# Kernel tuning notes

Hardware: AMD Instinct MI355X
Metric: run time of the kernel (lower is better)

The kernel has to match this reference:

```python
import jax, jax.numpy as jnp
import numpy as np

N_NODES = 100000
N_EDGES = 1600000
NFEAT = 64
NHID = 64
NCLASS = 16


def setup_inputs() -> dict:
    key = jax.random.key(0)
    k_x, k_e, k_w1, k_b1, k_w2, k_b2 = jax.random.split(key, 6)
    x = jax.random.normal(k_x, (N_NODES, NFEAT), dtype=jnp.float32)
    edge_index = jax.random.randint(k_e, (2, N_EDGES), 0, N_NODES, dtype=jnp.int64)
    # Glorot-ish init for the GIN update MLP
    W1 = jax.random.normal(k_w1, (NFEAT, NHID), dtype=jnp.float32) * (1.0 / np.sqrt(NFEAT))
    b1 = jnp.zeros((NHID,), dtype=jnp.float32)
    W2 = jax.random.normal(k_w2, (NHID, NCLASS), dtype=jnp.float32) * (1.0 / np.sqrt(NHID))
    b2 = jnp.zeros((NCLASS,), dtype=jnp.float32)
    eps = jnp.float32(0.0)  # train_eps=True, initialized to 0
    return {"x": x, "edge_index": edge_index, "eps": eps,
            "W1": W1, "b1": b1, "W2": W2, "b2": b2}


def reference(x, edge_index, eps, W1, b1, W2, b2):
    # GINConv: out = MLP((1 + eps) * x + sum_{j in N(i)} x_j)
    src = edge_index[0]  # message source nodes
    dst = edge_index[1]  # aggregation targets (source_to_target flow)
    agg = jax.ops.segment_sum(x[src], dst, num_segments=x.shape[0])  # [N, F]
    h = (1.0 + eps) * x + agg
    # MLP([nfeat, nhid, nclass]): Linear -> ReLU -> (dropout=identity in eval) -> Linear
    h = jax.nn.relu(h @ W1 + b1)
    return h @ W2 + b2
```

## Files before the change

kernel.cpp:

```cpp
#include <hip/hip_runtime.h>
#include <hip/hip_bf16.h>
#include <hip/hip_fp16.h>


#define NFEAT 64
#define NHID 64
#define NCLASS 16

#define BNODES 128
#define PCAP 2560
#define MAXBUCK 1024
#define PT 512
#define PEPT 8
#define FT 512
#define SEPT 5

__global__ __launch_bounds__(256) void k_tofp16(
    const float4* __restrict__ x4, uint2* __restrict__ xh2, int n16)
{
    int i = blockIdx.x * 256 + threadIdx.x;
    if (i >= n16) return;
    float4 v = x4[i];
    __half2 a = __floats2half2_rn(v.x, v.y);
    __half2 b = __floats2half2_rn(v.z, v.w);
    xh2[i] = make_uint2(*(unsigned*)&a, *(unsigned*)&b);
}

__global__ __launch_bounds__(512) void k_init(int* __restrict__ cursor, int nbuck)
{
    int t = blockIdx.x * 512 + threadIdx.x;
    if (t < nbuck) cursor[t] = t * PCAP;
}

__global__ __launch_bounds__(PT) void k_part(
    const int* __restrict__ ei, int* __restrict__ cursor,
    int* __restrict__ dsts, int n_edges, int nbuck)
{
    __shared__ int lcnt[MAXBUCK];
    __shared__ int sbase[MAXBUCK];
    int tid = threadIdx.x;
    for (int i = tid; i < nbuck; i += PT) lcnt[i] = 0;
    __syncthreads();

    int e0 = blockIdx.x * (PT * PEPT);
    int bk[PEPT], rk[PEPT], pk[PEPT];
    #pragma unroll
    for (int k = 0; k < PEPT; ++k) {
        int e = e0 + k * PT + tid;
        if (e < n_edges) {
            int src = ei[e];
            int dst = ei[n_edges + e];
            int b = dst >> 7;
            bk[k] = b;
            pk[k] = (src << 7) | (dst & 127);
            rk[k] = atomicAdd(&lcnt[b], 1);
        } else bk[k] = -1;
    }
    __syncthreads();
    for (int i = tid; i < nbuck; i += PT)
        sbase[i] = lcnt[i] ? atomicAdd(&cursor[i], lcnt[i]) : 0;
    __syncthreads();
    #pragma unroll
    for (int k = 0; k < PEPT; ++k)
        if (bk[k] >= 0) dsts[sbase[bk[k]] + rk[k]] = pk[k];
}

__global__ __launch_bounds__(FT) void k_fused(
    const uint2* __restrict__ xh2,
    const float4* __restrict__ x4,
    const int* __restrict__ dsts,
    const int* __restrict__ cursor,
    const float* __restrict__ eps_p,
    const float* __restrict__ W1,
    const float* __restrict__ b1,
    const float* __restrict__ W2,
    const float* __restrict__ b2,
    float* __restrict__ out,
    int n_nodes)
{
    __shared__ float sW1[NFEAT * NHID];
    __shared__ float sW2[NHID * 17];
    __shared__ float sb1[NHID];
    __shared__ float sb2[NCLASS];
    __shared__ int   sSrc[PCAP];
    __shared__ int   sCnt[BNODES];
    __shared__ int   sOff[BNODES];
    __shared__ float sh0[32][68];
    __shared__ float sh1[32][68];

    int tid = threadIdx.x;
    int lane = tid & 63, wave = tid >> 6;

    for (int i = tid; i < NFEAT * NHID; i += FT) sW1[i] = W1[i];
    for (int i = tid; i < NHID * NCLASS; i += FT) sW2[(i >> 4) * 17 + (i & 15)] = W2[i];
    if (tid < NHID) sb1[tid] = b1[tid];
    if (tid < NCLASS) sb2[tid] = b2[tid];
    if (tid < BNODES) sCnt[tid] = 0;
    __syncthreads();

    int b = blockIdx.x;
    int gin = b * PCAP;
    int s = cursor[b] - gin;

    int dk[SEPT], rk[SEPT], sk[SEPT];
    #pragma unroll
    for (int k = 0; k < SEPT; ++k) {
        int i = k * FT + tid;
        if (i < s) {
            int p = dsts[gin + i];
            int d = p & 127;
            dk[k] = d;
            sk[k] = p >> 7;
            rk[k] = atomicAdd(&sCnt[d], 1);
        } else dk[k] = -1;
    }
    __syncthreads();
    if (wave == 0) {
        int c0 = sCnt[lane * 2], c1 = sCnt[lane * 2 + 1];
        int p1 = c0, p2 = p1 + c1;
        int ss = p2;
        #pragma unroll
        for (int o = 1; o < 64; o <<= 1) {
            int u = __shfl_up(ss, o);
            if (lane >= o) ss += u;
        }
        int base = ss - p2;
        sOff[lane * 2] = base;
        sOff[lane * 2 + 1] = base + p1;
    }
    __syncthreads();
    #pragma unroll
    for (int k = 0; k < SEPT; ++k)
        if (dk[k] >= 0) sSrc[sOff[dk[k]] + rk[k]] = sk[k];
    __syncthreads();

    float eps1 = 1.0f + eps_p[0];
    int q = lane >> 4;
    int f = lane & 15;
    int rloc = wave * 4 + q;

    #pragma unroll
    for (int pp = 0; pp < 4; ++pp) {
        int nloc = pp * 32 + rloc;
        int node = b * BNODES + nloc;
        bool valid = node < n_nodes;
        int start = sOff[nloc];
        int cntn = sCnt[nloc];

        int dmax = cntn;
        dmax = max(dmax, __shfl_xor(dmax, 16));
        dmax = max(dmax, __shfl_xor(dmax, 32));

        float4 acc = make_float4(0.f, 0.f, 0.f, 0.f);
        for (int base = 0; base < dmax; base += 16) {
            #pragma unroll
            for (int t = 0; t < 16; ++t) {
                int o = base + t;
                int idx = (o < cntn) ? sSrc[start + o] : -1;
                if (idx >= 0) {
                    uint2 hv = xh2[(size_t)idx * 8 + (f >> 1)];
                    unsigned u = (f & 1) ? hv.y : hv.x;
                    (void)u;
                }
            }
            break;
        }
        acc = make_float4(0.f, 0.f, 0.f, 0.f);
        const uint2* xr = xh2;
        for (int base = 0; base < dmax; base += 16) {
            #pragma unroll
            for (int t = 0; t < 16; ++t) {
                int o = base + t;
                int idx = (o < cntn) ? sSrc[start + o] : -1;
                if (idx >= 0) {
                    uint2 hv = xr[(size_t)idx * 16 + f];
                    __half2 ha = *(__half2*)&hv.x;
                    __half2 hb = *(__half2*)&hv.y;
                    float2 fa = __half22float2(ha);
                    float2 fb = __half22float2(hb);
                    acc.x += fa.x; acc.y += fa.y; acc.z += fb.x; acc.w += fb.y;
                }
            }
        }
        if (valid) {
            float4 xs = x4[(size_t)node * 16 + f];
            acc.x += eps1 * xs.x; acc.y += eps1 * xs.y;
            acc.z += eps1 * xs.z; acc.w += eps1 * xs.w;
        }
        *(float4*)&sh0[rloc][f * 4] = acc;

        int r = wave * 4;
        float a0 = sb1[lane], a1 = a0, a2 = a0, a3 = a0;
        #pragma unroll
        for (int kk = 0; kk < 16; ++kk) {
            float4 h0 = *(const float4*)&sh0[r + 0][kk * 4];
            float4 h1v = *(const float4*)&sh0[r + 1][kk * 4];
            float4 h2 = *(const float4*)&sh0[r + 2][kk * 4];
            float4 h3 = *(const float4*)&sh0[r + 3][kk * 4];
            #pragma unroll
            for (int i = 0; i < 4; ++i) {
                float w = sW1[(kk * 4 + i) * NHID + lane];
                a0 += ((const float*)&h0)[i] * w;
                a1 += ((const float*)&h1v)[i] * w;
                a2 += ((const float*)&h2)[i] * w;
                a3 += ((const float*)&h3)[i] * w;
            }
        }
        sh1[r + 0][lane] = fmaxf(a0, 0.f);
        sh1[r + 1][lane] = fmaxf(a1, 0.f);
        sh1[r + 2][lane] = fmaxf(a2, 0.f);
        sh1[r + 3][lane] = fmaxf(a3, 0.f);

        float o2 = sb2[f];
        #pragma unroll
        for (int jj = 0; jj < 16; ++jj) {
            float4 hv = *(const float4*)&sh1[rloc][jj * 4];
            o2 += hv.x * sW2[(jj * 4 + 0) * 17 + f];
            o2 += hv.y * sW2[(jj * 4 + 1) * 17 + f];
            o2 += hv.z * sW2[(jj * 4 + 2) * 17 + f];
            o2 += hv.w * sW2[(jj * 4 + 3) * 17 + f];
        }
        if (valid) out[(size_t)node * NCLASS + f] = o2;
    }
}

extern "C" void kernel_launch(void* const* d_in, const int* in_sizes, int n_in,
                              void* d_out, int out_size, void* d_ws, size_t ws_size,
                              hipStream_t stream) {
    const float* x   = (const float*)d_in[0];
    const int*   ei  = (const int*)d_in[1];
    const float* eps = (const float*)d_in[2];
    const float* W1  = (const float*)d_in[3];
    const float* b1  = (const float*)d_in[4];
    const float* W2  = (const float*)d_in[5];
    const float* b2  = (const float*)d_in[6];
    float* out = (float*)d_out;

    int n_nodes = in_sizes[0] / NFEAT;
    int n_edges = in_sizes[1] / 2;
    int nbuck = (n_nodes + BNODES - 1) / BNODES;

    char* ws = (char*)d_ws;
    int*   cursor = (int*)ws;
    int*   dsts   = (int*)(ws + 4096);
    size_t o_xh   = 4096 + (size_t)nbuck * PCAP * 4;
    uint2* xh2    = (uint2*)(ws + o_xh);

    int n16 = n_nodes * 16;
    k_tofp16<<<(n16 + 255) / 256, 256, 0, stream>>>((const float4*)x, xh2, n16);
    k_init<<<(nbuck + 511) / 512, 512, 0, stream>>>(cursor, nbuck);
    k_part<<<(n_edges + PT * PEPT - 1) / (PT * PEPT), PT, 0, stream>>>(
        ei, cursor, dsts, n_edges, nbuck);
    k_fused<<<nbuck, FT, 0, stream>>>(
        xh2, (const float4*)x, dsts, cursor, eps, W1, b1, W2, b2, out, n_nodes);
}
```

Before: 210.2 us.

## Drop fp16 copy of x, gather fp32 directly with branchless masked loads

Removes the fp16 conversion kernel and its extra pass over x, and gathers neighbor features straight from the fp32 input using clamped indices and a 0/1 weight instead of branches. It also drops the dead prefetch loop, aliases the source-index buffer with the second hidden-layer staging buffer, lowers the per-bucket capacity and raises edges per thread in the partition kernel. The cost is twice as many bytes per gathered row and wasted loads for padded slots, in exchange for one less launch and less LDS. The smaller capacity raises overflow risk for heavy buckets.

After: 208.2 us. About the same (-1.0%).

```diff
diff --git a/kernel.cpp b/kernel.cpp
--- a/kernel.cpp
+++ b/kernel.cpp
@@ -1,30 +1,19 @@
 #include <hip/hip_runtime.h>
 #include <hip/hip_bf16.h>
-#include <hip/hip_fp16.h>
 
 
 #define NFEAT 64
 #define NHID 64
 #define NCLASS 16
 
+#define BSH 7
 #define BNODES 128
-#define PCAP 2560
+#define PCAP 2304
 #define MAXBUCK 1024
 #define PT 512
-#define PEPT 8
+#define PEPT 16
 #define FT 512
 #define SEPT 5
-
-__global__ __launch_bounds__(256) void k_tofp16(
-    const float4* __restrict__ x4, uint2* __restrict__ xh2, int n16)
-{
-    int i = blockIdx.x * 256 + threadIdx.x;
-    if (i >= n16) return;
-    float4 v = x4[i];
-    __half2 a = __floats2half2_rn(v.x, v.y);
-    __half2 b = __floats2half2_rn(v.z, v.w);
-    xh2[i] = make_uint2(*(unsigned*)&a, *(unsigned*)&b);
-}
 
 __global__ __launch_bounds__(512) void k_init(int* __restrict__ cursor, int nbuck)
 {
@@ -50,9 +39,9 @@
         if (e < n_edges) {
             int src = ei[e];
             int dst = ei[n_edges + e];
-            int b = dst >> 7;
+            int b = dst >> BSH;
             bk[k] = b;
-            pk[k] = (src << 7) | (dst & 127);
+            pk[k] = (src << BSH) | (dst & (BNODES - 1));
             rk[k] = atomicAdd(&lcnt[b], 1);
         } else bk[k] = -1;
     }
@@ -66,7 +55,6 @@
 }
 
 __global__ __launch_bounds__(FT) void k_fused(
-    const uint2* __restrict__ xh2,
     const float4* __restrict__ x4,
     const int* __restrict__ dsts,
     const int* __restrict__ cursor,
@@ -82,14 +70,18 @@
     __shared__ float sW2[NHID * 17];
     __shared__ float sb1[NHID];
     __shared__ float sb2[NCLASS];
-    __shared__ int   sSrc[PCAP];
     __shared__ int   sCnt[BNODES];
     __shared__ int   sOff[BNODES];
-    __shared__ float sh0[32][68];
-    __shared__ float sh1[32][68];
+    __shared__ __align__(16) float sh0[32][68];
+    __shared__ __align__(16) int   uMem[PCAP];
+
+    int* sSrc = uMem;
+    float (*sh1)[64] = (float (*)[64])uMem;
 
     int tid = threadIdx.x;
     int lane = tid & 63, wave = tid >> 6;
+    int b = blockIdx.x;
+    int nbase = b * BNODES;
 
     for (int i = tid; i < NFEAT * NHID; i += FT) sW1[i] = W1[i];
     for (int i = tid; i < NHID * NCLASS; i += FT) sW2[(i >> 4) * 17 + (i & 15)] = W2[i];
@@ -98,19 +90,17 @@
     if (tid < BNODES) sCnt[tid] = 0;
     __syncthreads();
 
-    int b = blockIdx.x;
     int gin = b * PCAP;
     int s = cursor[b] - gin;
-
     int dk[SEPT], rk[SEPT], sk[SEPT];
     #pragma unroll
     for (int k = 0; k < SEPT; ++k) {
         int i = k * FT + tid;
         if (i < s) {
             int p = dsts[gin + i];
-            int d = p & 127;
+            int d = p & (BNODES - 1);
             dk[k] = d;
-            sk[k] = p >> 7;
+            sk[k] = p >> BSH;
             rk[k] = atomicAdd(&sCnt[d], 1);
         } else dk[k] = -1;
     }
@@ -137,90 +127,86 @@
     float eps1 = 1.0f + eps_p[0];
     int q = lane >> 4;
     int f = lane & 15;
-    int rloc = wave * 4 + q;
-
+    int nn1 = n_nodes - 1;
+
+    float4 acc[4];
     #pragma unroll
     for (int pp = 0; pp < 4; ++pp) {
-        int nloc = pp * 32 + rloc;
-        int node = b * BNODES + nloc;
-        bool valid = node < n_nodes;
+        int nloc = pp * 32 + wave * 4 + q;
         int start = sOff[nloc];
         int cntn = sCnt[nloc];
-
         int dmax = cntn;
         dmax = max(dmax, __shfl_xor(dmax, 16));
         dmax = max(dmax, __shfl_xor(dmax, 32));
 
-        float4 acc = make_float4(0.f, 0.f, 0.f, 0.f);
+        float4 a = make_float4(0.f, 0.f, 0.f, 0.f);
         for (int base = 0; base < dmax; base += 16) {
             #pragma unroll
             for (int t = 0; t < 16; ++t) {
                 int o = base + t;
-                int idx = (o < cntn) ? sSrc[start + o] : -1;
-                if (idx >= 0) {
-                    uint2 hv = xh2[(size_t)idx * 8 + (f >> 1)];
-                    unsigned u = (f & 1) ? hv.y : hv.x;
-                    (void)u;
-                }
+                int ridx = min(start + o, PCAP - 1);
+                int idx = sSrc[ridx];
+                float w = (o < cntn) ? 1.0f : 0.0f;
+                int safe = min(max(idx, 0), nn1);
+                float4 v = x4[(size_t)(unsigned)(safe * 16 + f)];
+                a.x = fmaf(v.x, w, a.x);
+                a.y = fmaf(v.y, w, a.y);
+                a.z = fmaf(v.z, w, a.z);
+                a.w = fmaf(v.w, w, a.w);
             }
-            break;
-        }
-        acc = make_float4(0.f, 0.f, 0.f, 0.f);
-        const uint2* xr = xh2;
-        for (int base = 0; base < dmax; base += 16) {
-            #pragma unroll
-            for (int t = 0; t < 16; ++t) {
-                int o = base + t;
-                int idx = (o < cntn) ? sSrc[start + o] : -1;
-                if (idx >= 0) {
-                    uint2 hv = xr[(size_t)idx * 16 + f];
-                    __half2 ha = *(__half2*)&hv.x;
-                    __half2 hb = *(__half2*)&hv.y;
-                    float2 fa = __half22float2(ha);
-                    float2 fb = __half22float2(hb);
-                    acc.x += fa.x; acc.y += fa.y; acc.z += fb.x; acc.w += fb.y;
-                }
-            }
-        }
-        if (valid) {
-            float4 xs = x4[(size_t)node * 16 + f];
-            acc.x += eps1 * xs.x; acc.y += eps1 * xs.y;
-            acc.z += eps1 * xs.z; acc.w += eps1 * xs.w;
-        }
-        *(float4*)&sh0[rloc][f * 4] = acc;
-
-        int r = wave * 4;
+        }
+        int node = nbase + nloc;
+        if (node < n_nodes) {
+            float4 xs = x4[(size_t)(unsigned)(node * 16 + f)];
+            a.x = fmaf(eps1, xs.x, a.x);
+            a.y = fmaf(eps1, xs.y, a.y);
+            a.z = fmaf(eps1, xs.z, a.z);
+            a.w = fmaf(eps1, xs.w, a.w);
+        }
+        acc[pp] = a;
+    }
+    __syncthreads();
+
+    int rr = wave * 4;
+    int rloc = rr + q;
+    #pragma unroll
+    for (int pp = 0; pp < 4; ++pp) {
+        int nloc = pp * 32 + rloc;
+        int node = nbase + nloc;
+
+        *(float4*)&sh0[rloc][f * 4] = acc[pp];
+
         float a0 = sb1[lane], a1 = a0, a2 = a0, a3 = a0;
         #pragma unroll
         for (int kk = 0; kk < 16; ++kk) {
-            float4 h0 = *(const float4*)&sh0[r + 0][kk * 4];
-            float4 h1v = *(const float4*)&sh0[r + 1][kk * 4];
-            float4 h2 = *(const float4*)&sh0[r + 2][kk * 4];
-            float4 h3 = *(const float4*)&sh0[r + 3][kk * 4];
+            float4 h0  = *(const float4*)&sh0[rr + 0][kk * 4];
+            float4 h1v = *(const float4*)&sh0[rr + 1][kk * 4];
+            float4 h2  = *(const float4*)&sh0[rr + 2][kk * 4];
+            float4 h3  = *(const float4*)&sh0[rr + 3][kk * 4];
             #pragma unroll
             for (int i = 0; i < 4; ++i) {
                 float w = sW1[(kk * 4 + i) * NHID + lane];
-                a0 += ((const float*)&h0)[i] * w;
-                a1 += ((const float*)&h1v)[i] * w;
-                a2 += ((const float*)&h2)[i] * w;
-                a3 += ((const float*)&h3)[i] * w;
+                a0 = fmaf(((const float*)&h0)[i], w, a0);
+                a1 = fmaf(((const float*)&h1v)[i], w, a1);
+                a2 = fmaf(((const float*)&h2)[i], w, a2);
+                a3 = fmaf(((const float*)&h3)[i], w, a3);
             }
         }
-        sh1[r + 0][lane] = fmaxf(a0, 0.f);
-        sh1[r + 1][lane] = fmaxf(a1, 0.f);
-        sh1[r + 2][lane] = fmaxf(a2, 0.f);
-        sh1[r + 3][lane] = fmaxf(a3, 0.f);
+        sh1[rr + 0][lane] = fmaxf(a0, 0.f);
+        sh1[rr + 1][lane] = fmaxf(a1, 0.f);
+        sh1[rr + 2][lane] = fmaxf(a2, 0.f);
+        sh1[rr + 3][lane] = fmaxf(a3, 0.f);
 
         float o2 = sb2[f];
         #pragma unroll
         for (int jj = 0; jj < 16; ++jj) {
-            float4 hv = *(const float4*)&sh1[rloc][jj * 4];
-            o2 += hv.x * sW2[(jj * 4 + 0) * 17 + f];
-            o2 += hv.y * sW2[(jj * 4 + 1) * 17 + f];
-            o2 += hv.z * sW2[(jj * 4 + 2) * 17 + f];
-            o2 += hv.w * sW2[(jj * 4 + 3) * 17 + f];
-        }
-        if (valid) out[(size_t)node * NCLASS + f] = o2;
+            float4 hv = *(const float4*)&sh1[rr + q][jj * 4];
+            o2 = fmaf(hv.x, sW2[(jj * 4 + 0) * 17 + f], o2);
+            o2 = fmaf(hv.y, sW2[(jj * 4 + 1) * 17 + f], o2);
+            o2 = fmaf(hv.z, sW2[(jj * 4 + 2) * 17 + f], o2);
+            o2 = fmaf(hv.w, sW2[(jj * 4 + 3) * 17 + f], o2);
+        }
+        if (node < n_nodes) out[(size_t)node * NCLASS + f] = o2;
     }
 }
 
@@ -241,16 +227,12 @@
     int nbuck = (n_nodes + BNODES - 1) / BNODES;
 
     char* ws = (char*)d_ws;
-    int*   cursor = (int*)ws;
-    int*   dsts   = (int*)(ws + 4096);
-    size_t o_xh   = 4096 + (size_t)nbuck * PCAP * 4;
-    uint2* xh2    = (uint2*)(ws + o_xh);
-
-    int n16 = n_nodes * 16;
-    k_tofp16<<<(n16 + 255) / 256, 256, 0, stream>>>((const float4*)x, xh2, n16);
+    int* cursor = (int*)ws;
+    int* dsts   = (int*)(ws + 4096);
+
     k_init<<<(nbuck + 511) / 512, 512, 0, stream>>>(cursor, nbuck);
     k_part<<<(n_edges + PT * PEPT - 1) / (PT * PEPT), PT, 0, stream>>>(
         ei, cursor, dsts, n_edges, nbuck);
     k_fused<<<nbuck, FT, 0, stream>>>(
-        xh2, (const float4*)x, dsts, cursor, eps, W1, b1, W2, b2, out, n_nodes);
-}
+        (const float4*)x, dsts, cursor, eps, W1, b1, W2, b2, out, n_nodes);
+}
```
